# Kernel tuning notes

Hardware: AMD Instinct MI355X
Metric: run time of the kernel (lower is better)

Reference implementation:

```python
import jax, jax.numpy as jnp
import numpy as np

N_COMP = 36          # sdf_n_comp
GRID = 300           # gridSize per axis
SDF_DIM = 256
APP_DIM = 128
MULTIRES = 3         # sdf positional-encoding octaves -> 3 + 3*2*3 = 21 channels
N_PTS = 524288       # sample points per batch (~1024 rays x 512 samples)
EMB_CH = 3 + 3 * 2 * MULTIRES            # 21
IN_CH = EMB_CH + 3 * N_COMP              # 129
OUT_CH = 1 + APP_DIM                     # 129 (sdf + appearance feature)
INIT_RADIUS = 0.2


def setup_inputs() -> dict:
    key = jax.random.key(0)
    ks = jax.random.split(key, 6)
    xyz_sampled = jax.random.uniform(ks[0], (N_PTS, 3), jnp.float32) * 2.0 - 1.0
    # tensor-decomposition grids (stacked over the 3 VM planes)
    planes = jax.random.normal(ks[1], (3, N_COMP, GRID, GRID), jnp.float32) * 0.1
    lines = jax.random.normal(ks[2], (3, N_COMP, GRID), jnp.float32) * (1.0 / (N_COMP * 3))
    # sdf_mat MLP params, initialized per init_mlp()
    w1 = jax.random.normal(ks[3], (SDF_DIM, IN_CH), jnp.float32) * (np.sqrt(2.0) / np.sqrt(SDF_DIM))
    b1 = jnp.zeros((SDF_DIM,), jnp.float32)
    w2 = jax.random.normal(ks[4], (OUT_CH, SDF_DIM), jnp.float32) * 1e-4 + np.sqrt(np.pi) / np.sqrt(SDF_DIM)
    b2 = jnp.full((OUT_CH,), -INIT_RADIUS, jnp.float32)
    return {"xyz_sampled": xyz_sampled, "planes": planes, "lines": lines,
            "w1": w1, "b1": b1, "w2": w2, "b2": b2}


def _bilin2d(plane, x, y):
    """Bilinear grid_sample, align_corners=True. plane [C,H,W]; x,y [N] in [-1,1] -> [C,N]."""
    C, H, W = plane.shape
    fx = (x + 1.0) * 0.5 * (W - 1)
    fy = (y + 1.0) * 0.5 * (H - 1)
    x0 = jnp.clip(jnp.floor(fx).astype(jnp.int32), 0, W - 2)
    y0 = jnp.clip(jnp.floor(fy).astype(jnp.int32), 0, H - 2)
    tx = fx - x0
    ty = fy - y0
    v00 = plane[:, y0, x0]
    v01 = plane[:, y0, x0 + 1]
    v10 = plane[:, y0 + 1, x0]
    v11 = plane[:, y0 + 1, x0 + 1]
    return (v00 * (1 - tx) * (1 - ty) + v01 * tx * (1 - ty)
            + v10 * (1 - tx) * ty + v11 * tx * ty)


def _lin1d(line, z):
    """Linear grid_sample, align_corners=True. line [C,L]; z [N] in [-1,1] -> [C,N]."""
    C, L = line.shape
    fz = (z + 1.0) * 0.5 * (L - 1)
    z0 = jnp.clip(jnp.floor(fz).astype(jnp.int32), 0, L - 2)
    tz = fz - z0
    return line[:, z0] * (1 - tz) + line[:, z0 + 1] * tz


def _embed(x):
    """NeRF positional encoding, include_input, octaves 2^0..2^(MULTIRES-1). [N,3] -> [N,21]."""
    freqs = 2.0 ** jnp.arange(MULTIRES, dtype=x.dtype)
    ang = x[:, :, None] * freqs  # [N,3,MULTIRES]
    n = x.shape[0]
    return jnp.concatenate([x, jnp.sin(ang).reshape(n, -1), jnp.cos(ang).reshape(n, -1)], axis=-1)


def reference(xyz_sampled, planes, lines, w1, b1, w2, b2):
    # aabb = [-1,1]^3 -> normalization is identity, kept explicit for faithfulness
    xn = (xyz_sampled - (-1.0)) / 2.0 * 2.0 - 1.0
    # matMode=[[0,1],[0,2],[1,2]], vecMode=[2,1,0]
    px = jnp.stack([xn[:, 0], xn[:, 0], xn[:, 1]])  # [3,N] first plane coord
    py = jnp.stack([xn[:, 1], xn[:, 2], xn[:, 2]])  # [3,N] second plane coord
    pz = jnp.stack([xn[:, 2], xn[:, 1], xn[:, 0]])  # [3,N] line coord
    pf = jax.vmap(_bilin2d)(planes, px, py)         # [3,C,N]
    lf = jax.vmap(_lin1d)(lines, pz)                # [3,C,N]
    feat = (pf * lf).transpose(2, 0, 1).reshape(xn.shape[0], -1)  # [N, 3*C]
    mlp_in = jnp.concatenate([_embed(xyz_sampled), feat], axis=-1)  # [N, 129]
    h = jax.nn.softplus(100.0 * (mlp_in @ w1.T + b1)) / 100.0       # Softplus(beta=100)
    out = h @ w2.T + b2                                             # [N, 1+app_dim]
    return out
```

## Files before the change

kernel.cpp:

```cpp
#include <hip/hip_runtime.h>
#include <cstdint>
#include <cstddef>


using half2v  = __attribute__((ext_vector_type(2))) _Float16;
using half4   = __attribute__((ext_vector_type(4))) _Float16;
using half8   = __attribute__((ext_vector_type(8))) _Float16;
using floatx4 = __attribute__((ext_vector_type(4))) float;

#define NPTS    524288
#define GRES    300
#define NCOMP   36
#define NCP     40
#define SDFD    256
#define IN_CH   129
#define OUT_CH  129
#define TILE_M  64
#define S_INL   168
#define S_OUT   136

#define OFF_W1S 0
#define SZ_W1S  (5*4*256*8*2)
#define OFF_W2S (OFF_W1S + SZ_W1S)
#define SZ_W2S  (8*4*144*8*2)
#define OFF_LT  (OFF_W2S + SZ_W2S)
#define SZ_LT   (3*GRES*NCP*2)
#define OFF_PLT (OFF_LT + SZ_LT)
#define SZ_PLT  ((size_t)3*GRES*GRES*NCP*2)
#define NEED_FAST ((size_t)OFF_PLT + SZ_PLT)


__global__ void prep_planes_k(const float* __restrict__ planes, _Float16* __restrict__ pl_t) {
    int idx = blockIdx.x * 256 + threadIdx.x;
    if (idx >= 3 * GRES * GRES) return;
    int x = idx % GRES; int t = idx / GRES; int y = t % GRES; int m = t / GRES;
    _Float16* dst = pl_t + (size_t)idx * NCP;
    const float* src = planes + (size_t)m * NCOMP * GRES * GRES + (size_t)y * GRES + x;
    #pragma unroll
    for (int j = 0; j < 5; ++j) {
        half8 o;
        #pragma unroll
        for (int e = 0; e < 8; ++e) {
            int c = j * 8 + e;
            o[e] = (c < NCOMP) ? (_Float16)src[(size_t)c * GRES * GRES] : (_Float16)0.f;
        }
        *(half8*)(dst + j * 8) = o;
    }
}

#define NB_W1 ((5*4*256*8 + 255)/256)
#define NB_W2 ((8*4*144*8 + 255)/256)
#define NB_L  ((3*GRES + 255)/256)
__global__ void prep_small_k(const float* __restrict__ w1, const float* __restrict__ w2,
                             const float* __restrict__ lines,
                             _Float16* __restrict__ w1s, _Float16* __restrict__ w2s,
                             _Float16* __restrict__ l_t) {
    int b = blockIdx.x;
    if (b < NB_W1) {
        int t = b * 256 + threadIdx.x;
        int j = t & 7; int n = (t >> 3) & 255; int q = t >> 11;
        int k = q * 8 + j;
        float v = 0.f;
        if (k < 120) {
            int m = k / 40, c = k % 40;
            if (c < NCOMP) v = w1[n * IN_CH + 21 + m * NCOMP + c];
        } else if (k < 141) {
            v = w1[n * IN_CH + (k - 120)];
        }
        w1s[t] = (_Float16)v;
    } else if (b < NB_W1 + NB_W2) {
        int t = (b - NB_W1) * 256 + threadIdx.x;
        if (t >= 8*4*144*8) return;
        int j = t & 7; int r = t >> 3; int n = r % 144; int q = r / 144;
        int k = q * 8 + j;
        float v = (n < OUT_CH) ? w2[n * SDFD + k] : 0.f;
        w2s[t] = (_Float16)v;
    } else {
        int idx = (b - NB_W1 - NB_W2) * 256 + threadIdx.x;
        if (idx >= 3 * GRES) return;
        int z = idx % GRES; int m = idx / GRES;
        _Float16* dst = l_t + (size_t)idx * NCP;
        const float* src = lines + ((size_t)m * NCOMP) * GRES + z;
        #pragma unroll
        for (int c = 0; c < NCOMP; ++c) dst[c] = (_Float16)src[(size_t)c * GRES];
        dst[36] = dst[37] = dst[38] = dst[39] = (_Float16)0.f;
    }
}


__device__ __forceinline__ float softplus100(float z) {
    return fmaxf(z, 0.f) + __logf(1.f + __expf(-fabsf(z)));
}

__device__ __forceinline__ void plane_coords(int m, float X, float Y, float Z,
                                             int& x0, int& y0, int& z0,
                                             float& tx, float& ty, float& tz) {
    const float px = (m == 2) ? Y : X;
    const float py = (m == 0) ? Y : Z;
    const float pz = (m == 0) ? Z : ((m == 1) ? Y : X);
    float fx = (px + 1.f) * 0.5f * 299.f;
    float fy = (py + 1.f) * 0.5f * 299.f;
    float fz = (pz + 1.f) * 0.5f * 299.f;
    x0 = (int)floorf(fx); x0 = x0 < 0 ? 0 : (x0 > 298 ? 298 : x0);
    y0 = (int)floorf(fy); y0 = y0 < 0 ? 0 : (y0 > 298 ? 298 : y0);
    z0 = (int)floorf(fz); z0 = z0 < 0 ? 0 : (z0 > 298 ? 298 : z0);
    tx = fx - (float)x0; ty = fy - (float)y0; tz = fz - (float)z0;
}

__device__ __forceinline__ void embed_chunks(float X, float Y, float Z, half8 e[5]) {
    const float v3[3] = {X, Y, Z};
    _Float16 s[3][3], c[3][3];
    #pragma unroll
    for (int d = 0; d < 3; ++d) {
        float fm = 1.f;
        #pragma unroll
        for (int q = 0; q < 3; ++q) {
            const float a = v3[d] * fm;
            s[d][q] = (_Float16)__sinf(a);
            c[d][q] = (_Float16)__cosf(a);
            fm *= 2.f;
        }
    }
    const _Float16 z0 = (_Float16)0.f;
    e[0] = (half8){(_Float16)X, (_Float16)Y, (_Float16)Z, s[0][0], s[0][1], s[0][2], s[1][0], s[1][1]};
    e[1] = (half8){s[1][2], s[2][0], s[2][1], s[2][2], c[0][0], c[0][1], c[0][2], c[1][0]};
    e[2] = (half8){c[1][1], c[1][2], c[2][0], c[2][1], c[2][2], z0, z0, z0};
    e[3] = (half8){z0,z0,z0,z0,z0,z0,z0,z0};
    e[4] = (half8){z0,z0,z0,z0,z0,z0,z0,z0};
}

__device__ __forceinline__ half8 splat8(_Float16 v) {
    return (half8){v, v, v, v, v, v, v, v};
}


template <int FASTMODE>
__global__ __launch_bounds__(256, 3)
void tsdf_fused40_k(const float* __restrict__ xyz,
                    const float* __restrict__ planes, const float* __restrict__ lines,
                    const _Float16* __restrict__ pl_t, const _Float16* __restrict__ l_t,
                    const _Float16* __restrict__ w1s, const _Float16* __restrict__ w2s,
                    const float* __restrict__ b1, const float* __restrict__ b2,
                    float* __restrict__ out)
{
    __shared__ _Float16 lds_u[TILE_M * 272];
    _Float16* mlp_lds = lds_u;
    _Float16* h_lds   = lds_u;
    const int tid = threadIdx.x, blk = blockIdx.x;

    {
        const int task = tid & 15;
        const int pb4  = (tid >> 4) * 4;
        const int m    = task / 5;
        const int j    = task - m * 5;
        const float* xb = xyz + ((size_t)blk * TILE_M + pb4) * 3;
        const floatx4 xv0 = *(const floatx4*)(xb);
        const floatx4 xv1 = *(const floatx4*)(xb + 4);
        const floatx4 xv2 = *(const floatx4*)(xb + 8);
        #pragma unroll
        for (int g = 0; g < 4; ++g) {
            const int p = pb4 + g;
            const float X = (g == 0) ? xv0[0] : (g == 1) ? xv0[3] : (g == 2) ? xv1[2] : xv2[1];
            const float Y = (g == 0) ? xv0[1] : (g == 1) ? xv1[0] : (g == 2) ? xv1[3] : xv2[2];
            const float Z = (g == 0) ? xv0[2] : (g == 1) ? xv1[1] : (g == 2) ? xv2[0] : xv2[3];
            if (task < 15) {
                int x0, y0, z0; float tx, ty, tz;
                plane_coords(m, X, Y, Z, x0, y0, z0, tx, ty, tz);
                if (FASTMODE) {
                    const half8 W00 = splat8((_Float16)((1.f - tx) * (1.f - ty)));
                    const half8 W01 = splat8((_Float16)(tx * (1.f - ty)));
                    const half8 W10 = splat8((_Float16)((1.f - tx) * ty));
                    const half8 W11 = splat8((_Float16)(tx * ty));
                    const half8 WL0 = splat8((_Float16)(1.f - tz));
                    const half8 WL1 = splat8((_Float16)tz);
                    const _Float16* r0 = pl_t + ((size_t)(m * GRES + y0) * GRES + x0) * NCP + 8 * j;
                    const _Float16* r1 = r0 + (size_t)GRES * NCP;
                    const _Float16* lb = l_t + (size_t)(m * GRES + z0) * NCP + 8 * j;
                    const half8 v00 = *(const half8*)(r0);
                    const half8 v01 = *(const half8*)(r0 + NCP);
                    const half8 v10 = *(const half8*)(r1);
                    const half8 v11 = *(const half8*)(r1 + NCP);
                    const half8 l0  = *(const half8*)(lb);
                    const half8 l1  = *(const half8*)(lb + NCP);
                    const half8 pf = v00 * W00 + v01 * W01 + v10 * W10 + v11 * W11;
                    const half8 lf = l0 * WL0 + l1 * WL1;
                    *(half8*)&mlp_lds[p * S_INL + task * 8] = pf * lf;
                } else {
                    const float w00 = (1.f - tx) * (1.f - ty), w01 = tx * (1.f - ty);
                    const float w10 = (1.f - tx) * ty,         w11 = tx * ty;
                    const float lw0 = 1.f - tz, lw1 = tz;
                    half8 f;
                    #pragma unroll
                    for (int e = 0; e < 8; ++e) {
                        const int c = j * 8 + e;
                        float v = 0.f;
                        if (c < NCOMP) {
                            const float* pc = planes + ((size_t)(m * NCOMP + c) * GRES + y0) * GRES + x0;
                            const float* lc = lines + ((size_t)m * NCOMP + c) * GRES + z0;
                            const float pfv = pc[0] * w00 + pc[1] * w01 + pc[GRES] * w10 + pc[GRES + 1] * w11;
                            v = pfv * (lc[0] * lw0 + lc[1] * lw1);
                        }
                        f[e] = (_Float16)v;
                    }
                    *(half8*)&mlp_lds[p * S_INL + task * 8] = f;
                }
            } else {
                half8 e[5];
                embed_chunks(X, Y, Z, e);
                #pragma unroll
                for (int jj = 0; jj < 5; ++jj)
                    *(half8*)&mlp_lds[p * S_INL + (15 + jj) * 8] = e[jj];
            }
        }
    }
    __syncthreads();

    const int lane = tid & 63, wv = tid >> 6, l15 = lane & 15, quad = lane >> 4;

    floatx4 acc1[4][4];
    #pragma unroll
    for (int mt = 0; mt < 4; ++mt)
        #pragma unroll
        for (int nt = 0; nt < 4; ++nt)
            acc1[mt][nt] = (floatx4){0.f, 0.f, 0.f, 0.f};

    #pragma unroll
    for (int s = 0; s < 5; ++s) {
        half8 a[4], b[4];
        #pragma unroll
        for (int mt = 0; mt < 4; ++mt)
            a[mt] = *(const half8*)&mlp_lds[(mt * 16 + l15) * S_INL + s * 32 + quad * 8];
        #pragma unroll
        for (int nt = 0; nt < 4; ++nt)
            b[nt] = *(const half8*)(w1s + ((size_t)((s * 4 + quad) * 256) + wv * 64 + nt * 16 + l15) * 8);
        #pragma unroll
        for (int mt = 0; mt < 4; ++mt)
            #pragma unroll
            for (int nt = 0; nt < 4; ++nt)
                acc1[mt][nt] = __builtin_amdgcn_mfma_f32_16x16x32_f16(a[mt], b[nt], acc1[mt][nt], 0, 0, 0);
    }
    __syncthreads();

    #pragma unroll
    for (int nt = 0; nt < 4; ++nt) {
        const int n = wv * 64 + nt * 16 + l15;
        const float bias = b1[n];
        #pragma unroll
        for (int mt = 0; mt < 4; ++mt) {
            #pragma unroll
            for (int r = 0; r < 4; ++r) {
                const int rowh = mt * 16 + quad * 4 + r;
                const float z = 100.f * (acc1[mt][nt][r] + bias);
                h_lds[(rowh * 256 + n) ^ ((rowh & 7) << 3)] = (_Float16)(softplus100(z) * 0.01f);
            }
        }
    }
    __syncthreads();

    const int NTL = (wv == 0) ? 3 : 2;
    floatx4 acc2[4][3];
    #pragma unroll
    for (int mt = 0; mt < 4; ++mt)
        #pragma unroll
        for (int ntl = 0; ntl < 3; ++ntl)
            acc2[mt][ntl] = (floatx4){0.f, 0.f, 0.f, 0.f};

    #pragma unroll
    for (int s = 0; s < 8; ++s) {
        half8 a[4];
        #pragma unroll
        for (int mt = 0; mt < 4; ++mt) {
            const int rowh = mt * 16 + l15;
            a[mt] = *(const half8*)&h_lds[(rowh * 256 + s * 32 + quad * 8) ^ ((rowh & 7) << 3)];
        }
        #pragma unroll
        for (int ntl = 0; ntl < 3; ++ntl) {
            if (ntl < NTL) {
                const int ntg = wv + 4 * ntl;
                const half8 b = *(const half8*)(w2s + ((size_t)((s * 4 + quad) * 144) + ntg * 16 + l15) * 8);
                #pragma unroll
                for (int mt = 0; mt < 4; ++mt)
                    acc2[mt][ntl] = __builtin_amdgcn_mfma_f32_16x16x32_f16(a[mt], b, acc2[mt][ntl], 0, 0, 0);
            }
        }
    }

    __syncthreads();
    float* o_lds = (float*)lds_u;
    #pragma unroll
    for (int ntl = 0; ntl < 3; ++ntl) {
        if (ntl < NTL) {
            const int n = (wv + 4 * ntl) * 16 + l15;
            if (n < OUT_CH) {
                const float bias = b2[n];
                #pragma unroll
                for (int mt = 0; mt < 4; ++mt) {
                    #pragma unroll
                    for (int r = 0; r < 4; ++r)
                        o_lds[(mt * 16 + quad * 4 + r) * S_OUT + n] = acc2[mt][ntl][r] + bias;
                }
            }
        }
    }
    __syncthreads();
    float* oblk = out + (size_t)blk * TILE_M * OUT_CH;
    #pragma unroll
    for (int c = 0; c < 33; ++c) {
        const int idx = c * 256 + tid;
        if (idx < TILE_M * OUT_CH) {
            const int row = idx / 129;
            const int col = idx - row * 129;
            __builtin_nontemporal_store(o_lds[row * S_OUT + col], &oblk[idx]);
        }
    }
}


extern "C" void kernel_launch(void* const* d_in, const int* in_sizes, int n_in,
                              void* d_out, int out_size, void* d_ws, size_t ws_size,
                              hipStream_t stream) {
    const float* xyz    = (const float*)d_in[0];
    const float* planes = (const float*)d_in[1];
    const float* lines  = (const float*)d_in[2];
    const float* w1     = (const float*)d_in[3];
    const float* b1     = (const float*)d_in[4];
    const float* w2     = (const float*)d_in[5];
    const float* b2     = (const float*)d_in[6];
    float* out = (float*)d_out;
    char* ws = (char*)d_ws;

    _Float16* w1s  = (_Float16*)(ws + OFF_W1S);
    _Float16* w2s  = (_Float16*)(ws + OFF_W2S);
    _Float16* l_t  = (_Float16*)(ws + OFF_LT);
    _Float16* pl_t = (_Float16*)(ws + OFF_PLT);

    const bool fast = (ws_size >= NEED_FAST);

    prep_small_k<<<NB_W1 + NB_W2 + NB_L, 256, 0, stream>>>(w1, w2, lines, w1s, w2s, l_t);

    if (fast) {
        prep_planes_k<<<(3 * GRES * GRES + 255) / 256, 256, 0, stream>>>(planes, pl_t);
        tsdf_fused40_k<1><<<NPTS / TILE_M, 256, 0, stream>>>(
            xyz, planes, lines, pl_t, l_t, w1s, w2s, b1, b2, out);
    } else {
        tsdf_fused40_k<0><<<NPTS / TILE_M, 256, 0, stream>>>(
            xyz, planes, lines, pl_t, l_t, w1s, w2s, b1, b2, out);
    }
}
```

Before: 498.3 us.

## Sort sample points by Morton cell to improve plane-gather locality

Adds a counting sort of points into a 32^3 Morton-ordered grid (zero, histogram, scan, scatter kernels) and has the fused kernel process points in sorted order through a permutation. Input coordinates are gathered through the permutation and output rows are scattered back to their original positions. The intent is to make the random bilinear plane gathers more cache-local. In exchange it adds four extra launches, atomic traffic, a serial single-block scan, and uncoalesced per-row output writes.

Measured after the change: 610.4 us. +22.5%, slower.

```diff
diff --git a/kernel.cpp b/kernel.cpp
--- a/kernel.cpp
+++ b/kernel.cpp
@@ -18,6 +18,7 @@
 #define TILE_M  64
 #define S_INL   168
 #define S_OUT   136
+#define NCELL   32768
 
 #define OFF_W1S 0
 #define SZ_W1S  (5*4*256*8*2)
@@ -25,7 +26,13 @@
 #define SZ_W2S  (8*4*144*8*2)
 #define OFF_LT  (OFF_W2S + SZ_W2S)
 #define SZ_LT   (3*GRES*NCP*2)
-#define OFF_PLT (OFF_LT + SZ_LT)
+#define OFF_HIST (OFF_LT + SZ_LT + 64)
+#define SZ_HIST (NCELL*4)
+#define OFF_CUR (OFF_HIST + SZ_HIST)
+#define SZ_CUR  (NCELL*4)
+#define OFF_PERM (OFF_CUR + SZ_CUR)
+#define SZ_PERM (NPTS*4)
+#define OFF_PLT (OFF_PERM + SZ_PERM)
 #define SZ_PLT  ((size_t)3*GRES*GRES*NCP*2)
 #define NEED_FAST ((size_t)OFF_PLT + SZ_PLT)
 
@@ -88,6 +95,58 @@
 }
 
 
+__device__ __forceinline__ uint32_t spread5(uint32_t a) {
+    a &= 31u;
+    a = (a | (a << 8)) & 0x100Fu;
+    a = (a | (a << 4)) & 0x10C3u;
+    a = (a | (a << 2)) & 0x1249u;
+    return a;
+}
+
+__device__ __forceinline__ uint32_t cell_code(float X, float Y, float Z) {
+    int cx = (int)((X + 1.f) * 16.f); cx = cx < 0 ? 0 : (cx > 31 ? 31 : cx);
+    int cy = (int)((Y + 1.f) * 16.f); cy = cy < 0 ? 0 : (cy > 31 ? 31 : cy);
+    int cz = (int)((Z + 1.f) * 16.f); cz = cz < 0 ? 0 : (cz > 31 ? 31 : cz);
+    return spread5((uint32_t)cx) | (spread5((uint32_t)cy) << 1) | (spread5((uint32_t)cz) << 2);
+}
+
+__global__ void zero_k(uint32_t* __restrict__ p) {
+    p[blockIdx.x * 256 + threadIdx.x] = 0u;
+}
+
+__global__ void hist_k(const float* __restrict__ xyz, uint32_t* __restrict__ hist) {
+    int i = blockIdx.x * 256 + threadIdx.x;
+    atomicAdd(&hist[cell_code(xyz[i*3], xyz[i*3+1], xyz[i*3+2])], 1u);
+}
+
+__global__ void scan_k(const uint32_t* __restrict__ hist, uint32_t* __restrict__ cur) {
+    __shared__ uint32_t part[256];
+    const int t = threadIdx.x;
+    uint32_t s = 0;
+    for (int i = 0; i < NCELL/256; ++i) s += hist[t * (NCELL/256) + i];
+    part[t] = s;
+    __syncthreads();
+    if (t == 0) {
+        uint32_t a = 0;
+        for (int i = 0; i < 256; ++i) { uint32_t v = part[i]; part[i] = a; a += v; }
+    }
+    __syncthreads();
+    uint32_t a = part[t];
+    for (int i = 0; i < NCELL/256; ++i) {
+        uint32_t v = hist[t * (NCELL/256) + i];
+        cur[t * (NCELL/256) + i] = a;
+        a += v;
+    }
+}
+
+__global__ void scat_k(const float* __restrict__ xyz, uint32_t* __restrict__ cur,
+                       uint32_t* __restrict__ perm) {
+    int i = blockIdx.x * 256 + threadIdx.x;
+    uint32_t idx = atomicAdd(&cur[cell_code(xyz[i*3], xyz[i*3+1], xyz[i*3+2])], 1u);
+    perm[idx] = (uint32_t)i;
+}
+
+
 __device__ __forceinline__ float softplus100(float z) {
     return fmaxf(z, 0.f) + __logf(1.f + __expf(-fabsf(z)));
 }
@@ -141,28 +200,37 @@
                     const _Float16* __restrict__ pl_t, const _Float16* __restrict__ l_t,
                     const _Float16* __restrict__ w1s, const _Float16* __restrict__ w2s,
                     const float* __restrict__ b1, const float* __restrict__ b2,
+                    const uint32_t* __restrict__ perm,
                     float* __restrict__ out)
 {
     __shared__ _Float16 lds_u[TILE_M * 272];
+    __shared__ uint32_t perm_s[TILE_M];
     _Float16* mlp_lds = lds_u;
     _Float16* h_lds   = lds_u;
+    float*    xyz_s   = (float*)&lds_u[10752];
     const int tid = threadIdx.x, blk = blockIdx.x;
+
+    if (tid < TILE_M)
+        perm_s[tid] = perm ? perm[(size_t)blk * TILE_M + tid]
+                           : (uint32_t)(blk * TILE_M + tid);
+    __syncthreads();
+    if (tid < TILE_M * 3) {
+        const int pt = tid / 3, c = tid - pt * 3;
+        xyz_s[tid] = xyz[(size_t)perm_s[pt] * 3 + c];
+    }
+    __syncthreads();
 
     {
         const int task = tid & 15;
         const int pb4  = (tid >> 4) * 4;
         const int m    = task / 5;
         const int j    = task - m * 5;
-        const float* xb = xyz + ((size_t)blk * TILE_M + pb4) * 3;
-        const floatx4 xv0 = *(const floatx4*)(xb);
-        const floatx4 xv1 = *(const floatx4*)(xb + 4);
-        const floatx4 xv2 = *(const floatx4*)(xb + 8);
         #pragma unroll
         for (int g = 0; g < 4; ++g) {
             const int p = pb4 + g;
-            const float X = (g == 0) ? xv0[0] : (g == 1) ? xv0[3] : (g == 2) ? xv1[2] : xv2[1];
-            const float Y = (g == 0) ? xv0[1] : (g == 1) ? xv1[0] : (g == 2) ? xv1[3] : xv2[2];
-            const float Z = (g == 0) ? xv0[2] : (g == 1) ? xv1[1] : (g == 2) ? xv2[0] : xv2[3];
+            const float X = xyz_s[p * 3 + 0];
+            const float Y = xyz_s[p * 3 + 1];
+            const float Z = xyz_s[p * 3 + 2];
             if (task < 15) {
                 int x0, y0, z0; float tx, ty, tz;
                 plane_coords(m, X, Y, Z, x0, y0, z0, tx, ty, tz);
@@ -303,15 +371,14 @@
         }
     }
     __syncthreads();
-    float* oblk = out + (size_t)blk * TILE_M * OUT_CH;
-    #pragma unroll
-    for (int c = 0; c < 33; ++c) {
-        const int idx = c * 256 + tid;
-        if (idx < TILE_M * OUT_CH) {
-            const int row = idx / 129;
-            const int col = idx - row * 129;
-            __builtin_nontemporal_store(o_lds[row * S_OUT + col], &oblk[idx]);
-        }
+    #pragma unroll
+    for (int rr = 0; rr < 16; ++rr) {
+        const int row = wv * 16 + rr;
+        float* dst = out + (size_t)perm_s[row] * OUT_CH;
+        const float* src = &o_lds[row * S_OUT];
+        dst[lane] = src[lane];
+        dst[64 + lane] = src[64 + lane];
+        if (lane == 0) dst[128] = src[128];
     }
 }
 
@@ -332,6 +399,9 @@
     _Float16* w1s  = (_Float16*)(ws + OFF_W1S);
     _Float16* w2s  = (_Float16*)(ws + OFF_W2S);
     _Float16* l_t  = (_Float16*)(ws + OFF_LT);
+    uint32_t* hist = (uint32_t*)(ws + OFF_HIST);
+    uint32_t* cur  = (uint32_t*)(ws + OFF_CUR);
+    uint32_t* perm = (uint32_t*)(ws + OFF_PERM);
     _Float16* pl_t = (_Float16*)(ws + OFF_PLT);
 
     const bool fast = (ws_size >= NEED_FAST);
@@ -340,10 +410,14 @@
 
     if (fast) {
         prep_planes_k<<<(3 * GRES * GRES + 255) / 256, 256, 0, stream>>>(planes, pl_t);
+        zero_k<<<NCELL / 256, 256, 0, stream>>>(hist);
+        hist_k<<<NPTS / 256, 256, 0, stream>>>(xyz, hist);
+        scan_k<<<1, 256, 0, stream>>>(hist, cur);
+        scat_k<<<NPTS / 256, 256, 0, stream>>>(xyz, cur, perm);
         tsdf_fused40_k<1><<<NPTS / TILE_M, 256, 0, stream>>>(
-            xyz, planes, lines, pl_t, l_t, w1s, w2s, b1, b2, out);
+            xyz, planes, lines, pl_t, l_t, w1s, w2s, b1, b2, perm, out);
     } else {
         tsdf_fused40_k<0><<<NPTS / TILE_M, 256, 0, stream>>>(
-            xyz, planes, lines, pl_t, l_t, w1s, w2s, b1, b2, out);
-    }
-}
+            xyz, planes, lines, pl_t, l_t, w1s, w2s, b1, b2, nullptr, out);
+    }
+}
```
